# Kernel optimization log

Hardware: AMD Instinct MI355X
Metric: run time of the kernel (lower is better)

Reference implementation:

```python
import jax, jax.numpy as jnp
import numpy as np

N_NODES = 100000
N_EDGES = 1600000
IN_CH = 128
OUT_CH = 64


def setup_inputs() -> dict:
    key = jax.random.key(0)
    k1, k2, k3 = jax.random.split(key, 3)
    x = jax.random.normal(k1, (N_NODES, IN_CH), dtype=jnp.float32)
    edge_index = jax.random.randint(k2, (2, N_EDGES), 0, N_NODES, dtype=jnp.int32)
    # Glorot-style init for the GCN weight
    W = jax.random.normal(k3, (IN_CH, OUT_CH), dtype=jnp.float32) * (1.0 / np.sqrt(IN_CH))
    b = jnp.zeros((OUT_CH,), dtype=jnp.float32)
    return {"x": x, "edge_index": edge_index, "W": W, "b": b}


def reference(x, edge_index, W, b):
    # GCNConv (PyG semantics): linear transform, add self loops,
    # symmetric deg^{-1/2} normalization, scatter-add aggregation, bias; then ReLU.
    n = x.shape[0]
    h = x @ W  # [N, out]

    loops = jnp.arange(n, dtype=edge_index.dtype)
    row = jnp.concatenate([edge_index[0], loops])  # source nodes
    col = jnp.concatenate([edge_index[1], loops])  # target nodes

    deg = jax.ops.segment_sum(jnp.ones_like(col, dtype=h.dtype), col, num_segments=n)
    deg_inv_sqrt = jnp.where(deg > 0, jax.lax.rsqrt(jnp.maximum(deg, 1e-12)), 0.0)
    norm = deg_inv_sqrt[row] * deg_inv_sqrt[col]  # [E+N]

    msg = h[row] * norm[:, None]  # gather + scale
    out = jax.ops.segment_sum(msg, col, num_segments=n)  # scatter-add
    return jax.nn.relu(out + b)
```

## Files before the change

kernel.cpp:

```cpp
#include <hip/hip_runtime.h>
#include <hip/hip_fp16.h>

#define INC 128
#define OUTC 64
#define MAXBUK 512
#define CAP 6144
#define FCH 3200

typedef __attribute__((ext_vector_type(8))) short short8;
typedef __attribute__((ext_vector_type(4))) float f32x4;

__device__ __forceinline__ ushort f2bf(float f) {
    union { float f; unsigned u; } v; v.f = f;
    unsigned r = v.u + 0x7FFF + ((v.u >> 16) & 1);
    return (ushort)(r >> 16);
}

__global__ __launch_bounds__(512) void buk_fill_kernel(const int* __restrict__ rowi,
                                                       const int* __restrict__ coli,
                                                       int* __restrict__ cursor,
                                                       int* __restrict__ packed,
                                                       int E, int nbuk, int per) {
    __shared__ int lcnt[512];
    __shared__ int sc[512];
    __shared__ int lbase[512];
    __shared__ int sp[FCH];
    __shared__ ushort sb[FCH];
    int tid = threadIdx.x;
    int c0 = blockIdx.x * per;
    int c1 = min(E, c0 + per);
    lcnt[tid] = 0;
    __syncthreads();
    for (int e = c0 + tid; e < c1; e += 512)
        atomicAdd(&lcnt[coli[e] >> 8], 1);
    __syncthreads();
    int v = lcnt[tid];
    sc[tid] = v;
    __syncthreads();
    #pragma unroll
    for (int off = 1; off < 512; off <<= 1) {
        int t = (tid >= off) ? sc[tid - off] : 0;
        __syncthreads();
        sc[tid] += t;
        __syncthreads();
    }
    int ex = sc[tid] - v;
    int gb = 0;
    if (v) gb = atomicAdd(&cursor[tid], v);
    lbase[tid] = gb - ex;
    lcnt[tid] = ex;
    __syncthreads();
    for (int e = c0 + tid; e < c1; e += 512) {
        int s = rowi[e], d = coli[e];
        int bk = d >> 8;
        int pos = atomicAdd(&lcnt[bk], 1);
        sp[pos] = (s << 8) | (d & 255);
        sb[pos] = (ushort)bk;
    }
    __syncthreads();
    int m = c1 - c0;
    for (int t = tid; t < m; t += 512) {
        int bk = sb[t];
        int p = lbase[bk] + t;
        if (p < CAP)
            packed[(size_t)bk * CAP + p] = sp[t];
    }
}

__global__ __launch_bounds__(1024) void deg_kernel(const int* __restrict__ packed,
                                                   const int* __restrict__ cursor,
                                                   float* __restrict__ dinv, int n) {
    __shared__ int cnt[256];
    int k = blockIdx.x, tid = threadIdx.x;
    if (tid < 256) cnt[tid] = 0;
    __syncthreads();
    int m = min(cursor[k], CAP);
    const int* pk = packed + (size_t)k * CAP;
    for (int e = tid; e < m; e += 1024)
        atomicAdd(&cnt[pk[e] & 255], 1);
    __syncthreads();
    int node = (k << 8) + tid;
    if (tid < 256 && node < n) dinv[node] = rsqrtf(1.0f + (float)cnt[tid]);
}

#define WT_STRIDE 136
__global__ __launch_bounds__(256) void gemm_kernel(
        const float* __restrict__ x, const float* __restrict__ W,
        const float* __restrict__ dinv, __half2* __restrict__ g2, int n) {
    __shared__ ushort WT[OUTC * WT_STRIDE];
    int tid = threadIdx.x;
    #pragma unroll
    for (int i = 0; i < 8; ++i) {
        int idx4 = tid + i * 256;
        float4 v = ((const float4*)W)[idx4];
        int e = idx4 * 4;
        int k = e >> 6, nn = e & 63;
        WT[(nn + 0) * WT_STRIDE + k] = f2bf(v.x);
        WT[(nn + 1) * WT_STRIDE + k] = f2bf(v.y);
        WT[(nn + 2) * WT_STRIDE + k] = f2bf(v.z);
        WT[(nn + 3) * WT_STRIDE + k] = f2bf(v.w);
    }
    __syncthreads();

    int w = tid >> 6, lane = tid & 63;
    int m = lane & 15, quad = lane >> 4;
    int rbase = blockIdx.x * 128 + w * 32;

    short8 afrag[2][4];
    #pragma unroll
    for (int rt = 0; rt < 2; ++rt) {
        int row = rbase + rt * 16 + m;
        #pragma unroll
        for (int kc = 0; kc < 4; ++kc) {
            float4 v0 = make_float4(0.f, 0.f, 0.f, 0.f), v1 = v0;
            if (row < n) {
                const float* p = x + (size_t)row * INC + kc * 32 + quad * 8;
                v0 = *(const float4*)p;
                v1 = *(const float4*)(p + 4);
            }
            short8 a;
            a[0] = (short)f2bf(v0.x); a[1] = (short)f2bf(v0.y);
            a[2] = (short)f2bf(v0.z); a[3] = (short)f2bf(v0.w);
            a[4] = (short)f2bf(v1.x); a[5] = (short)f2bf(v1.y);
            a[6] = (short)f2bf(v1.z); a[7] = (short)f2bf(v1.w);
            afrag[rt][kc] = a;
        }
    }

    f32x4 acc[2][4];
    #pragma unroll
    for (int rt = 0; rt < 2; ++rt)
        #pragma unroll
        for (int nt = 0; nt < 4; ++nt)
            acc[rt][nt] = (f32x4){0.f, 0.f, 0.f, 0.f};

    #pragma unroll
    for (int nt = 0; nt < 4; ++nt) {
        #pragma unroll
        for (int kc = 0; kc < 4; ++kc) {
            short8 bf = *(const short8*)&WT[(nt * 16 + m) * WT_STRIDE + kc * 32 + quad * 8];
            acc[0][nt] = __builtin_amdgcn_mfma_f32_16x16x32_bf16(afrag[0][kc], bf, acc[0][nt], 0, 0, 0);
            acc[1][nt] = __builtin_amdgcn_mfma_f32_16x16x32_bf16(afrag[1][kc], bf, acc[1][nt], 0, 0, 0);
        }
    }

    #pragma unroll
    for (int rt = 0; rt < 2; ++rt) {
        #pragma unroll
        for (int reg = 0; reg < 4; ++reg) {
            int r2 = rbase + rt * 16 + quad * 4 + reg;
            if (r2 < n) {
                float di = dinv[r2];
                #pragma unroll
                for (int nt = 0; nt < 2; ++nt)
                    g2[(size_t)r2 * 32 + nt * 16 + m] =
                        __floats2half2_rn(acc[rt][nt][reg] * di, acc[rt][nt + 2][reg] * di);
            }
        }
    }
}

__global__ __launch_bounds__(1024) void agg_kernel(const int* __restrict__ packed,
                                                   const int* __restrict__ cursor,
                                                   const __half2* __restrict__ g2,
                                                   const float* __restrict__ b,
                                                   float* __restrict__ out, int n) {
    __shared__ int cnt[256];
    __shared__ int sc[256];
    __shared__ int cur[256];
    __shared__ int lcsr[CAP];
    int k = blockIdx.x, tid = threadIdx.x;
    int r0 = k << 8;
    if (tid < 256) cnt[tid] = 0;
    __syncthreads();
    int m = min(cursor[k], CAP);
    const int* pk = packed + (size_t)k * CAP;
    int pe[(CAP + 1023) / 1024];
    int ne = 0;
    for (int e = tid; e < m; e += 1024) {
        int p = pk[e];
        pe[ne++] = p;
        atomicAdd(&cnt[p & 255], 1);
    }
    __syncthreads();
    int c = (tid < 256) ? cnt[tid] : 0;
    if (tid < 256) sc[tid] = c;
    __syncthreads();
    #pragma unroll
    for (int off = 1; off < 256; off <<= 1) {
        int t = (tid >= off && tid < 256) ? sc[tid - off] : 0;
        __syncthreads();
        if (tid < 256) sc[tid] += t;
        __syncthreads();
    }
    if (tid < 256) cur[tid] = sc[tid] - c;
    __syncthreads();
    for (int i = 0; i < ne; ++i) {
        int p = pe[i];
        int pos = atomicAdd(&cur[p & 255], 1);
        lcsr[pos] = (int)(((unsigned)p) >> 8);
    }
    __syncthreads();

    int w = tid >> 6, lane = tid & 63;
    int l = lane & 31, half = lane >> 5;
    const __half2* gl = g2 + l;
    float bx = b[l], by = b[l + 32];
    for (int cl = w; cl < 256; cl += 16) {
        int e1 = sc[cl];
        int nd = cnt[cl];
        int j = e1 - nd;
        float ax = 0.f, ay = 0.f;
        for (; j + 16 <= e1; j += 16) {
            int s0 = lcsr[j + half];
            int s1 = lcsr[j + 2 + half];
            int s2 = lcsr[j + 4 + half];
            int s3 = lcsr[j + 6 + half];
            int s4 = lcsr[j + 8 + half];
            int s5 = lcsr[j + 10 + half];
            int s6 = lcsr[j + 12 + half];
            int s7 = lcsr[j + 14 + half];
            float2 f0 = __half22float2(gl[(size_t)s0 * 32]);
            float2 f1 = __half22float2(gl[(size_t)s1 * 32]);
            float2 f2 = __half22float2(gl[(size_t)s2 * 32]);
            float2 f3 = __half22float2(gl[(size_t)s3 * 32]);
            float2 f4 = __half22float2(gl[(size_t)s4 * 32]);
            float2 f5 = __half22float2(gl[(size_t)s5 * 32]);
            float2 f6 = __half22float2(gl[(size_t)s6 * 32]);
            float2 f7 = __half22float2(gl[(size_t)s7 * 32]);
            ax += ((f0.x + f1.x) + (f2.x + f3.x)) + ((f4.x + f5.x) + (f6.x + f7.x));
            ay += ((f0.y + f1.y) + (f2.y + f3.y)) + ((f4.y + f5.y) + (f6.y + f7.y));
        }
        if (j + 8 <= e1) {
            int s0 = lcsr[j + half];
            int s1 = lcsr[j + 2 + half];
            int s2 = lcsr[j + 4 + half];
            int s3 = lcsr[j + 6 + half];
            float2 f0 = __half22float2(gl[(size_t)s0 * 32]);
            float2 f1 = __half22float2(gl[(size_t)s1 * 32]);
            float2 f2 = __half22float2(gl[(size_t)s2 * 32]);
            float2 f3 = __half22float2(gl[(size_t)s3 * 32]);
            ax += (f0.x + f1.x) + (f2.x + f3.x);
            ay += (f0.y + f1.y) + (f2.y + f3.y);
            j += 8;
        }
        for (; j + 2 <= e1; j += 2) {
            int s = lcsr[j + half];
            float2 f = __half22float2(gl[(size_t)s * 32]);
            ax += f.x; ay += f.y;
        }
        if (j < e1 && half == 0) {
            int s = lcsr[j];
            float2 f = __half22float2(gl[(size_t)s * 32]);
            ax += f.x; ay += f.y;
        }
        ax += __shfl_xor(ax, 32);
        ay += __shfl_xor(ay, 32);
        int node = r0 + cl;
        if (half == 0 && node < n) {
            float2 s = __half22float2(gl[(size_t)node * 32]);
            float di = rsqrtf(1.0f + (float)nd);
            out[(size_t)node * OUTC + l]      = fmaxf((ax + s.x) * di + bx, 0.f);
            out[(size_t)node * OUTC + 32 + l] = fmaxf((ay + s.y) * di + by, 0.f);
        }
    }
}

extern "C" void kernel_launch(void* const* d_in, const int* in_sizes, int n_in,
                              void* d_out, int out_size, void* d_ws, size_t ws_size,
                              hipStream_t stream) {
    const float* x  = (const float*)d_in[0];
    const int*   ei = (const int*)d_in[1];
    const float* W  = (const float*)d_in[2];
    const float* b  = (const float*)d_in[3];
    float* out = (float*)d_out;

    int n = in_sizes[0] / INC;
    int E = in_sizes[1] / 2;
    const int* rowi = ei;
    const int* coli = ei + E;

    int nbuk = (n + 255) >> 8;
    int n_pad = ((n + 255) / 256) * 256;

    char* ws = (char*)d_ws;
    int*     cursor = (int*)ws;                  ws += (size_t)MAXBUK * 4;
    float*   dinv   = (float*)ws;                ws += (size_t)n_pad * 4;
    int*     packed = (int*)ws;                  ws += (size_t)nbuk * CAP * 4;
    __half2* g2     = (__half2*)ws;

    int fblocks = 512;
    int per = (E + fblocks - 1) / fblocks;

    (void)hipMemsetAsync(cursor, 0, (size_t)MAXBUK * 4, stream);
    buk_fill_kernel<<<fblocks, 512, 0, stream>>>(rowi, coli, cursor, packed, E, nbuk, per);
    deg_kernel<<<nbuk, 1024, 0, stream>>>(packed, cursor, dinv, n);
    gemm_kernel<<<(n + 127) / 128, 256, 0, stream>>>(x, W, dinv, g2, n);
    agg_kernel<<<nbuk, 1024, 0, stream>>>(packed, cursor, g2, b, out, n);
}
```

Measured before the change: 169.3 us.

## Fuse degree counting into GEMM kernel and double bucket-fill block count

Removes the separate degree kernel and dinv buffer. Each GEMM block now scans its 256-node bucket's packed edge list, counts the in-degrees of its own 128 rows in shared memory, and computes rsqrt inline. This saves a kernel launch and a global round-trip, but each bucket list is read twice, once by each of the two GEMM blocks covering it. The fill kernel also uses 1024 blocks with a smaller per-block chunk (FCH 1664) for more parallelism in the bucketing pass.

```diff
diff --git a/kernel.cpp b/kernel.cpp
--- a/kernel.cpp
+++ b/kernel.cpp
@@ -5,7 +5,7 @@
 #define OUTC 64
 #define MAXBUK 512
 #define CAP 6144
-#define FCH 3200
+#define FCH 1664
 
 typedef __attribute__((ext_vector_type(8))) short short8;
 typedef __attribute__((ext_vector_type(4))) float f32x4;
@@ -67,28 +67,15 @@
     }
 }
 
-__global__ __launch_bounds__(1024) void deg_kernel(const int* __restrict__ packed,
-                                                   const int* __restrict__ cursor,
-                                                   float* __restrict__ dinv, int n) {
-    __shared__ int cnt[256];
-    int k = blockIdx.x, tid = threadIdx.x;
-    if (tid < 256) cnt[tid] = 0;
-    __syncthreads();
-    int m = min(cursor[k], CAP);
-    const int* pk = packed + (size_t)k * CAP;
-    for (int e = tid; e < m; e += 1024)
-        atomicAdd(&cnt[pk[e] & 255], 1);
-    __syncthreads();
-    int node = (k << 8) + tid;
-    if (tid < 256 && node < n) dinv[node] = rsqrtf(1.0f + (float)cnt[tid]);
-}
-
 #define WT_STRIDE 136
 __global__ __launch_bounds__(256) void gemm_kernel(
         const float* __restrict__ x, const float* __restrict__ W,
-        const float* __restrict__ dinv, __half2* __restrict__ g2, int n) {
+        const int* __restrict__ packed, const int* __restrict__ cursor,
+        __half2* __restrict__ g2, int n) {
     __shared__ ushort WT[OUTC * WT_STRIDE];
+    __shared__ int cnt[128];
     int tid = threadIdx.x;
+    if (tid < 128) cnt[tid] = 0;
     #pragma unroll
     for (int i = 0; i < 8; ++i) {
         int idx4 = tid + i * 256;
@@ -102,14 +89,27 @@
     }
     __syncthreads();
 
+    int rbase = blockIdx.x * 128;
+    int bucket = rbase >> 8;
+    int off = rbase & 255;
+
+    {
+        int m = min(cursor[bucket], CAP);
+        const int* pk = packed + (size_t)bucket * CAP;
+        for (int e = tid; e < m; e += 256) {
+            int r = (pk[e] & 255) - off;
+            if ((unsigned)r < 128u) atomicAdd(&cnt[r], 1);
+        }
+    }
+
     int w = tid >> 6, lane = tid & 63;
     int m = lane & 15, quad = lane >> 4;
-    int rbase = blockIdx.x * 128 + w * 32;
+    int rw = rbase + w * 32;
 
     short8 afrag[2][4];
     #pragma unroll
     for (int rt = 0; rt < 2; ++rt) {
-        int row = rbase + rt * 16 + m;
+        int row = rw + rt * 16 + m;
         #pragma unroll
         for (int kc = 0; kc < 4; ++kc) {
             float4 v0 = make_float4(0.f, 0.f, 0.f, 0.f), v1 = v0;
@@ -144,13 +144,15 @@
         }
     }
 
+    __syncthreads();
+
     #pragma unroll
     for (int rt = 0; rt < 2; ++rt) {
         #pragma unroll
         for (int reg = 0; reg < 4; ++reg) {
-            int r2 = rbase + rt * 16 + quad * 4 + reg;
+            int r2 = rw + rt * 16 + quad * 4 + reg;
             if (r2 < n) {
-                float di = dinv[r2];
+                float di = rsqrtf(1.0f + (float)cnt[r2 - rbase]);
                 #pragma unroll
                 for (int nt = 0; nt < 2; ++nt)
                     g2[(size_t)r2 * 32 + nt * 16 + m] =
@@ -281,20 +283,17 @@
     const int* coli = ei + E;
 
     int nbuk = (n + 255) >> 8;
-    int n_pad = ((n + 255) / 256) * 256;
 
     char* ws = (char*)d_ws;
     int*     cursor = (int*)ws;                  ws += (size_t)MAXBUK * 4;
-    float*   dinv   = (float*)ws;                ws += (size_t)n_pad * 4;
     int*     packed = (int*)ws;                  ws += (size_t)nbuk * CAP * 4;
     __half2* g2     = (__half2*)ws;
 
-    int fblocks = 512;
+    int fblocks = 1024;
     int per = (E + fblocks - 1) / fblocks;
 
     (void)hipMemsetAsync(cursor, 0, (size_t)MAXBUK * 4, stream);
     buk_fill_kernel<<<fblocks, 512, 0, stream>>>(rowi, coli, cursor, packed, E, nbuk, per);
-    deg_kernel<<<nbuk, 1024, 0, stream>>>(packed, cursor, dinv, n);
-    gemm_kernel<<<(n + 127) / 128, 256, 0, stream>>>(x, W, dinv, g2, n);
+    gemm_kernel<<<(n + 127) / 128, 256, 0, stream>>>(x, W, packed, cursor, g2, n);
     agg_kernel<<<nbuk, 1024, 0, stream>>>(packed, cursor, g2, b, out, n);
 }
```

New measurement: 181.8 us. 1.07x slower.
